# Optimization experiments

Measured on AMD Instinct MI355X. Metric: run time of the kernel, lower is better.

The kernel has to match this reference:

```python
import jax, jax.numpy as jnp
import numpy as np

NUM_EXPERTS = 8
HIDDEN = 2048
INTER = 4096
TOKENS = 4096
TOP_K = 2


def setup_inputs() -> dict:
    key = jax.random.key(0)
    ks = jax.random.split(key, 6)
    x = jax.random.normal(ks[0], (TOKENS, HIDDEN), dtype=jnp.float32)
    expert_weights = jax.random.uniform(ks[1], (TOKENS, TOP_K), dtype=jnp.float32)
    expert_indices = jax.random.randint(ks[2], (TOKENS, TOP_K), 0, NUM_EXPERTS)
    # kaiming_uniform-ish init for stacked expert weights
    b1 = float(np.sqrt(6.0 / HIDDEN))
    b2 = float(np.sqrt(6.0 / INTER))
    w1_stacked = jax.random.uniform(ks[3], (NUM_EXPERTS, HIDDEN, INTER), minval=-b1, maxval=b1, dtype=jnp.float32)
    w2_stacked = jax.random.uniform(ks[4], (NUM_EXPERTS, INTER, HIDDEN), minval=-b2, maxval=b2, dtype=jnp.float32)
    w3_stacked = jax.random.uniform(ks[5], (NUM_EXPERTS, HIDDEN, INTER), minval=-b1, maxval=b1, dtype=jnp.float32)
    return {
        "x": x,
        "expert_weights": expert_weights,
        "w1_stacked": w1_stacked,
        "w2_stacked": w2_stacked,
        "w3_stacked": w3_stacked,
        "expert_indices": expert_indices,
        "num_experts_per_tok": TOP_K,
    }


def reference(x, expert_weights, w1_stacked, w2_stacked, w3_stacked, expert_indices, num_experts_per_tok):
    # out[t] = sum_k expert_weights[t,k] * SwiGLU_FFN_{expert_indices[t,k]}(x[t])
    # Loop over the small fixed expert set; masked weighted combine per expert.
    num_experts = w1_stacked.shape[0]
    out = jnp.zeros_like(x)
    for e in range(num_experts):
        gate = jax.nn.silu(x @ w1_stacked[e])          # [T, I]
        up = x @ w3_stacked[e]                          # [T, I]
        y = (gate * up) @ w2_stacked[e]                 # [T, H]
        # per-token routing weight for expert e (sum over top-k slots)
        w_e = jnp.sum(jnp.where(expert_indices == e, expert_weights, 0.0), axis=1)  # [T]
        out = out + w_e[:, None] * y
    return out
```

## Files before the change

### kernel.cpp

```cpp
#include <hip/hip_runtime.h>
#include <hip/hip_bf16.h>
#include <cstdint>

#define T_TOKENS 4096
#define HID      2048
#define INTER    4096
#define NEXP     8
#define TOPK     2
#define NPAIRS   (T_TOKENS * TOPK)
#define BM 128
#define BN 128
#define BK 32
#define MAXROWS  (NPAIRS + NEXP * BM)
#define NRB1     64

typedef __attribute__((ext_vector_type(8))) short   short8;
typedef __attribute__((ext_vector_type(4))) float   f32x4;
typedef __attribute__((ext_vector_type(8))) ushort  ushort8v;

static __device__ __forceinline__ ushort f2bf(float f) {
    __hip_bfloat16 b = __float2bfloat16(f);
    return __builtin_bit_cast(ushort, b);
}

typedef const __attribute__((address_space(1))) unsigned char ga_u8;
typedef __attribute__((address_space(3))) unsigned char       la_u8;
static __device__ __forceinline__ void gl_lds16(const void* g, void* l) {
    __builtin_amdgcn_global_load_lds((ga_u8*)g, (la_u8*)l, 16, 0, 0);
}

__global__ void route_kernel(const int* __restrict__ eidx,
                             const float* __restrict__ ew,
                             int* __restrict__ cnt, int* __restrict__ pbase,
                             int* __restrict__ tokl, float* __restrict__ wgtl,
                             int* __restrict__ pairrow) {
    __shared__ int s_cnt[NEXP];
    __shared__ int s_pos[NEXP];
    __shared__ int s_base[NEXP];
    int tid = threadIdx.x;
    if (tid < NEXP) { s_cnt[tid] = 0; s_pos[tid] = 0; }
    __syncthreads();
    for (int p = tid; p < NPAIRS; p += blockDim.x)
        atomicAdd(&s_cnt[eidx[p]], 1);
    __syncthreads();
    if (tid == 0) {
        int b = 0;
        for (int e = 0; e < NEXP; ++e) {
            s_base[e] = b;
            cnt[e]    = s_cnt[e];
            pbase[e]  = b;
            b += (s_cnt[e] + BM - 1) / BM * BM;
        }
        pbase[NEXP] = b;
    }
    __syncthreads();
    for (int p = tid; p < NPAIRS; p += blockDim.x) {
        int e   = eidx[p];
        int pos = atomicAdd(&s_pos[e], 1);
        int row = s_base[e] + pos;
        tokl[row]  = p >> 1;
        wgtl[row]  = ew[p];
        pairrow[p] = row;
    }
}

__global__ __launch_bounds__(256) void cvt_x_kernel(const float* __restrict__ x,
                                                    ushort* __restrict__ xbf) {
    int i = (blockIdx.x * 256 + threadIdx.x) * 8;
    float4 a = *reinterpret_cast<const float4*>(x + i);
    float4 b = *reinterpret_cast<const float4*>(x + i + 4);
    ushort8v o;
    o[0] = f2bf(a.x); o[1] = f2bf(a.y); o[2] = f2bf(a.z); o[3] = f2bf(a.w);
    o[4] = f2bf(b.x); o[5] = f2bf(b.y); o[6] = f2bf(b.z); o[7] = f2bf(b.w);
    *reinterpret_cast<ushort8v*>(xbf + i) = o;
}

__global__ __launch_bounds__(256) void transpose_cvt_kernel(
        const float* __restrict__ src, ushort* __restrict__ dst,
        int K, int N, int c0, int CN, long estride) {
    int ez = blockIdx.z;
    const float* s = src + (size_t)ez * estride;
    ushort* d = dst + (size_t)ez * CN * K;
    int nb = blockIdx.x * 64 + c0;
    int kb = blockIdx.y * 64;
    __shared__ ushort t[64][72];
    int tid = threadIdx.x;
    int kr = tid >> 2;
    int ns = tid & 3;
    #pragma unroll
    for (int p = 0; p < 4; ++p) {
        int f = ns + p * 4;
        float4 v = *reinterpret_cast<const float4*>(&s[(size_t)(kb + kr) * N + nb + f * 4]);
        t[f * 4 + 0][kr] = f2bf(v.x);
        t[f * 4 + 1][kr] = f2bf(v.y);
        t[f * 4 + 2][kr] = f2bf(v.z);
        t[f * 4 + 3][kr] = f2bf(v.w);
    }
    __syncthreads();
    int nr = tid >> 2;
    #pragma unroll
    for (int p = 0; p < 2; ++p) {
        int ks = ((tid & 3) + p * 4) * 8;
        ushort8v v8 = *reinterpret_cast<const ushort8v*>(&t[nr][ks]);
        *reinterpret_cast<ushort8v*>(&d[(size_t)(nb - c0 + nr) * K + kb + ks]) = v8;
    }
}

#define SWZV(r) (((r) & 3) ^ (((r) >> 2) & 3))

#define F1_LDSB 24576
__global__ __launch_bounds__(256, 2) void ffn1_kernel(
        const ushort* __restrict__ xbf,
        const ushort* __restrict__ wT1, const ushort* __restrict__ wT3,
        const int* __restrict__ cnt, const int* __restrict__ pbase,
        const int* __restrict__ tokl, ushort* __restrict__ h,
        int e0, int CN, int c0) {
    int d = blockIdx.x;
    int xcd = d & 7, q = d >> 3;
    int gq = q / NRB1, rb = q % NRB1;
    int ncb = CN >> 7;
    int g = gq * 8 + xcd;
    int ez = g / ncb, cb = g - ez * ncb;
    int e = e0 + ez;
    int ce = cnt[e];
    int r0 = rb * BM;
    if (r0 >= ce) return;
    int base = pbase[e];

    __shared__ ushort ldsbuf[2 * F1_LDSB / 2];
    int tid = threadIdx.x, lane = tid & 63, wid = tid >> 6;
    int wr = (wid >> 1) * 64, wc = (wid & 1) * 64;

    int t0 = wid * 32 + (lane >> 2);
    int t1 = t0 + 16;
    int sw0 = (((lane & 3) ^ SWZV(t0)) << 4);
    int sw1 = (((lane & 3) ^ SWZV(t1)) << 4);
    int cr0 = r0 + t0, cr1 = r0 + t1;
    const char* aS0 = (const char*)(xbf + (size_t)tokl[base + (cr0 < ce ? cr0 : 0)] * HID) + sw0;
    const char* aS1 = (const char*)(xbf + (size_t)tokl[base + (cr1 < ce ? cr1 : 0)] * HID) + sw1;
    const ushort* B1g = wT1 + ((size_t)ez * CN + (size_t)cb * 128) * HID;
    const ushort* B3g = wT3 + ((size_t)ez * CN + (size_t)cb * 128) * HID;
    const char* b1S0 = (const char*)(B1g + (size_t)t0 * HID) + sw0;
    const char* b1S1 = (const char*)(B1g + (size_t)t1 * HID) + sw1;
    const char* b3S0 = (const char*)(B3g + (size_t)t0 * HID) + sw0;
    const char* b3S1 = (const char*)(B3g + (size_t)t1 * HID) + sw1;

    char* Lb = (char*)ldsbuf;
    int dst0 = wid * 2048;

    int vl = SWZV(lane & 15);
    int fs = (((lane >> 4) ^ vl) << 4);
    int aoff[4], boff[4];
    #pragma unroll
    for (int i = 0; i < 4; ++i) {
        aoff[i] = (wr + i * 16 + (lane & 15)) * 64 + fs;
        boff[i] = (wc + i * 16 + (lane & 15)) * 64 + fs;
    }

    f32x4 accg[4][4], accu[4][4];
    #pragma unroll
    for (int i = 0; i < 4; ++i)
        #pragma unroll
        for (int j = 0; j < 4; ++j) { accg[i][j] = (f32x4)0.f; accu[i][j] = (f32x4)0.f; }

    auto stage = [&](int buf, int t) {
        char* L = Lb + buf * F1_LDSB;
        int adv = t * 64;
        gl_lds16(aS0 + adv,  L + dst0);
        gl_lds16(aS1 + adv,  L + dst0 + 1024);
        gl_lds16(b1S0 + adv, L + 8192 + dst0);
        gl_lds16(b1S1 + adv, L + 8192 + dst0 + 1024);
        gl_lds16(b3S0 + adv, L + 16384 + dst0);
        gl_lds16(b3S1 + adv, L + 16384 + dst0 + 1024);
    };

    stage(0, 0);
    __syncthreads();
    const int NT = HID / BK;
    for (int t = 0; t < NT; ++t) {
        int cur = t & 1;
        if (t + 1 < NT) stage(cur ^ 1, t + 1);
        const char* L = Lb + cur * F1_LDSB;
        short8 af[4];
        #pragma unroll
        for (int mi = 0; mi < 4; ++mi)
            af[mi] = *reinterpret_cast<const short8*>(L + aoff[mi]);
        #pragma unroll
        for (int ni = 0; ni < 4; ++ni) {
            short8 b1 = *reinterpret_cast<const short8*>(L + 8192 + boff[ni]);
            short8 b3 = *reinterpret_cast<const short8*>(L + 16384 + boff[ni]);
            #pragma unroll
            for (int mi = 0; mi < 4; ++mi) {
                accg[mi][ni] = __builtin_amdgcn_mfma_f32_16x16x32_bf16(af[mi], b1, accg[mi][ni], 0, 0, 0);
                accu[mi][ni] = __builtin_amdgcn_mfma_f32_16x16x32_bf16(af[mi], b3, accu[mi][ni], 0, 0, 0);
            }
        }
        __syncthreads();
    }

    int hcol = c0 + cb * 128 + wc + (lane & 15);
    #pragma unroll
    for (int mi = 0; mi < 4; ++mi) {
        #pragma unroll
        for (int q2 = 0; q2 < 4; ++q2) {
            int r = r0 + wr + mi * 16 + (lane >> 4) * 4 + q2;
            if (r >= ce) continue;
            ushort* hp = h + (size_t)(base + r) * INTER + hcol;
            #pragma unroll
            for (int ni = 0; ni < 4; ++ni) {
                float gg = accg[mi][ni][q2];
                float uu = accu[mi][ni][q2];
                float s = gg / (1.f + __expf(-gg));
                hp[ni * 16] = f2bf(s * uu);
            }
        }
    }
}

#define F2_LDSB 16384
__global__ __launch_bounds__(256, 3) void ffn2_kernel(
        const ushort* __restrict__ h,
        const ushort* __restrict__ wT2,
        const int* __restrict__ cnt, const int* __restrict__ pbase,
        const float* __restrict__ wgtl, ushort* __restrict__ y,
        int e0, int CN, int c0) {
    int d = blockIdx.x;
    int xcd = d & 7, q = d >> 3;
    int gq = q / NRB1, rb = q % NRB1;
    int ncb = CN >> 7;
    int g = gq * 8 + xcd;
    int ez = g / ncb, cb = g - ez * ncb;
    int e = e0 + ez;
    int ce = cnt[e];
    int r0 = rb * BM;
    if (r0 >= ce) return;
    int base = pbase[e];

    __shared__ ushort ldsbuf[2 * F2_LDSB / 2];
    int tid = threadIdx.x, lane = tid & 63, wid = tid >> 6;
    int wr = (wid >> 1) * 64, wc = (wid & 1) * 64;

    int t0 = wid * 32 + (lane >> 2);
    int t1 = t0 + 16;
    int sw0 = (((lane & 3) ^ SWZV(t0)) << 4);
    int sw1 = (((lane & 3) ^ SWZV(t1)) << 4);
    int cr0 = r0 + t0, cr1 = r0 + t1;
    const char* aS0 = (const char*)(h + (size_t)(base + (cr0 < ce ? cr0 : 0)) * INTER) + sw0;
    const char* aS1 = (const char*)(h + (size_t)(base + (cr1 < ce ? cr1 : 0)) * INTER) + sw1;
    const ushort* Bg = wT2 + ((size_t)ez * CN + (size_t)cb * 128) * INTER;
    const char* bS0 = (const char*)(Bg + (size_t)t0 * INTER) + sw0;
    const char* bS1 = (const char*)(Bg + (size_t)t1 * INTER) + sw1;

    char* Lb = (char*)ldsbuf;
    int dst0 = wid * 2048;

    int vl = SWZV(lane & 15);
    int fs = (((lane >> 4) ^ vl) << 4);
    int aoff[4], boff[4];
    #pragma unroll
    for (int i = 0; i < 4; ++i) {
        aoff[i] = (wr + i * 16 + (lane & 15)) * 64 + fs;
        boff[i] = (wc + i * 16 + (lane & 15)) * 64 + fs;
    }

    f32x4 acc[4][4];
    #pragma unroll
    for (int i = 0; i < 4; ++i)
        #pragma unroll
        for (int j = 0; j < 4; ++j) acc[i][j] = (f32x4)0.f;

    auto stage = [&](int buf, int t) {
        char* L = Lb + buf * F2_LDSB;
        int adv = t * 64;
        gl_lds16(aS0 + adv, L + dst0);
        gl_lds16(aS1 + adv, L + dst0 + 1024);
        gl_lds16(bS0 + adv, L + 8192 + dst0);
        gl_lds16(bS1 + adv, L + 8192 + dst0 + 1024);
    };

    stage(0, 0);
    __syncthreads();
    const int NT = INTER / BK;
    for (int t = 0; t < NT; ++t) {
        int cur = t & 1;
        if (t + 1 < NT) stage(cur ^ 1, t + 1);
        const char* L = Lb + cur * F2_LDSB;
        short8 af[4];
        #pragma unroll
        for (int mi = 0; mi < 4; ++mi)
            af[mi] = *reinterpret_cast<const short8*>(L + aoff[mi]);
        #pragma unroll
        for (int ni = 0; ni < 4; ++ni) {
            short8 b = *reinterpret_cast<const short8*>(L + 8192 + boff[ni]);
            #pragma unroll
            for (int mi = 0; mi < 4; ++mi)
                acc[mi][ni] = __builtin_amdgcn_mfma_f32_16x16x32_bf16(af[mi], b, acc[mi][ni], 0, 0, 0);
        }
        __syncthreads();
    }

    int ycol = c0 + cb * 128 + wc + (lane & 15);
    #pragma unroll
    for (int mi = 0; mi < 4; ++mi) {
        #pragma unroll
        for (int q2 = 0; q2 < 4; ++q2) {
            int r = r0 + wr + mi * 16 + (lane >> 4) * 4 + q2;
            if (r >= ce) continue;
            float wv = wgtl[base + r];
            ushort* yp = y + (size_t)(base + r) * HID + ycol;
            #pragma unroll
            for (int ni = 0; ni < 4; ++ni)
                yp[ni * 16] = f2bf(wv * acc[mi][ni][q2]);
        }
    }
}

__global__ __launch_bounds__(256) void combine_kernel(
        const ushort* __restrict__ y, const int* __restrict__ pairrow,
        float* __restrict__ out) {
    int t = blockIdx.x;
    const ushort* y0 = y + (size_t)pairrow[2 * t] * HID;
    const ushort* y1 = y + (size_t)pairrow[2 * t + 1] * HID;
    float* op = out + (size_t)t * HID;
    int c = threadIdx.x * 8;
    uint4 a = *reinterpret_cast<const uint4*>(y0 + c);
    uint4 b = *reinterpret_cast<const uint4*>(y1 + c);
    const uint* au = reinterpret_cast<const uint*>(&a);
    const uint* bu = reinterpret_cast<const uint*>(&b);
    #pragma unroll
    for (int i = 0; i < 4; ++i) {
        float alo = __builtin_bit_cast(float, au[i] << 16);
        float ahi = __builtin_bit_cast(float, au[i] & 0xffff0000u);
        float blo = __builtin_bit_cast(float, bu[i] << 16);
        float bhi = __builtin_bit_cast(float, bu[i] & 0xffff0000u);
        op[c + 2 * i]     = alo + blo;
        op[c + 2 * i + 1] = ahi + bhi;
    }
}

extern "C" void kernel_launch(void* const* d_in, const int* in_sizes, int n_in,
                              void* d_out, int out_size, void* d_ws, size_t ws_size,
                              hipStream_t stream) {
    (void)in_sizes; (void)n_in; (void)out_size;
    const float* x   = (const float*)d_in[0];
    const float* ew  = (const float*)d_in[1];
    const float* w1  = (const float*)d_in[2];
    const float* w2  = (const float*)d_in[3];
    const float* w3  = (const float*)d_in[4];
    const int*  eidx = (const int*)d_in[5];
    float* out = (float*)d_out;

    int*   cnt     = (int*)d_ws;
    int*   pbase   = cnt + 8;
    int*   tokl    = cnt + 32;
    float* wgtl    = (float*)(tokl + MAXROWS);
    int*   pairrow = (int*)(wgtl + MAXROWS);
    ushort* xbf = (ushort*)((((uintptr_t)(pairrow + NPAIRS)) + 255) & ~(uintptr_t)255);
    ushort* h   = xbf + (size_t)T_TOKENS * HID;
    ushort* y   = h + (size_t)MAXROWS * INTER;
    ushort* region = y + (size_t)MAXROWS * HID;
    size_t region_bytes = ws_size - ((char*)region - (char*)d_ws);

    route_kernel<<<1, 256, 0, stream>>>(eidx, ew, cnt, pbase, tokl, wgtl, pairrow);
    cvt_x_kernel<<<T_TOKENS * HID / 8 / 256, 256, 0, stream>>>(x, xbf);

    const size_t per_e1 = (size_t)2 * INTER * HID * 2;
    const size_t per_e2 = (size_t)HID * INTER * 2;

    if (region_bytes >= per_e1) {
        int EG = (int)(region_bytes / per_e1); if (EG > 8) EG = 8;
        for (int g = 0; g < NEXP; g += EG) {
            int ne = (NEXP - g < EG) ? (NEXP - g) : EG;
            ushort* wt1 = region;
            ushort* wt3 = region + (size_t)ne * INTER * HID;
            transpose_cvt_kernel<<<dim3(INTER / 64, HID / 64, ne), 256, 0, stream>>>(
                w1 + (size_t)g * HID * INTER, wt1, HID, INTER, 0, INTER, (long)HID * INTER);
            transpose_cvt_kernel<<<dim3(INTER / 64, HID / 64, ne), 256, 0, stream>>>(
                w3 + (size_t)g * HID * INTER, wt3, HID, INTER, 0, INTER, (long)HID * INTER);
            ffn1_kernel<<<NRB1 * ne * (INTER / BN), 256, 0, stream>>>(
                xbf, wt1, wt3, cnt, pbase, tokl, h, g, INTER, 0);
        }
    } else {
        const int CN = 1024;
        for (int e = 0; e < NEXP; ++e) {
            for (int c = 0; c < INTER; c += CN) {
                ushort* wt1 = region;
                ushort* wt3 = region + (size_t)CN * HID;
                transpose_cvt_kernel<<<dim3(CN / 64, HID / 64, 1), 256, 0, stream>>>(
                    w1 + (size_t)e * HID * INTER, wt1, HID, INTER, c, CN, (long)HID * INTER);
                transpose_cvt_kernel<<<dim3(CN / 64, HID / 64, 1), 256, 0, stream>>>(
                    w3 + (size_t)e * HID * INTER, wt3, HID, INTER, c, CN, (long)HID * INTER);
                ffn1_kernel<<<NRB1 * (CN / BN), 256, 0, stream>>>(
                    xbf, wt1, wt3, cnt, pbase, tokl, h, e, CN, c);
            }
        }
    }

    if (region_bytes >= per_e2) {
        int EG = (int)(region_bytes / per_e2); if (EG > 8) EG = 8;
        for (int g = 0; g < NEXP; g += EG) {
            int ne = (NEXP - g < EG) ? (NEXP - g) : EG;
            ushort* wt2 = region;
            transpose_cvt_kernel<<<dim3(HID / 64, INTER / 64, ne), 256, 0, stream>>>(
                w2 + (size_t)g * INTER * HID, wt2, INTER, HID, 0, HID, (long)INTER * HID);
            ffn2_kernel<<<NRB1 * ne * (HID / BN), 256, 0, stream>>>(
                h, wt2, cnt, pbase, wgtl, y, g, HID, 0);
        }
    } else {
        const int CN = 1024;
        for (int e = 0; e < NEXP; ++e) {
            for (int c = 0; c < HID; c += CN) {
                ushort* wt2 = region;
                transpose_cvt_kernel<<<dim3(CN / 64, INTER / 64, 1), 256, 0, stream>>>(
                    w2 + (size_t)e * INTER * HID, wt2, INTER, HID, c, CN, (long)INTER * HID);
                ffn2_kernel<<<NRB1 * (CN / BN), 256, 0, stream>>>(
                    h, wt2, cnt, pbase, wgtl, y, e, CN, c);
            }
        }
    }

    combine_kernel<<<T_TOKENS, 256, 0, stream>>>(y, pairrow, out);
}
```

Measured before the change: 855.2 us.

## Enlarge MoE GEMM tiles, interleave async loads with MFMA phases, fuse combine via atomics

Both expert GEMM kernels move to 256x128x64 tiles with 512-thread blocks and a larger double-buffered LDS. Global-to-LDS loads for the next k-step are split into chunks placed between MFMA phases, with explicit vmcnt waits, scheduling barriers and s_setprio around the math. The separate combine kernel and y buffer are removed: ffn2 applies the routing weight and atomically adds into the zero-initialised output. This trades more LDS per block (lower occupancy) and float-atomic traffic for better data reuse, better load/compute overlap and one less kernel plus its memory round-trip.

```diff
diff --git a/kernel.cpp b/kernel.cpp
--- a/kernel.cpp
+++ b/kernel.cpp
@@ -8,11 +8,11 @@
 #define NEXP     8
 #define TOPK     2
 #define NPAIRS   (T_TOKENS * TOPK)
-#define BM 128
+#define BM 256
 #define BN 128
-#define BK 32
+#define BK 64
 #define MAXROWS  (NPAIRS + NEXP * BM)
-#define NRB1     64
+#define NRB2     32
 
 typedef __attribute__((ext_vector_type(8))) short   short8;
 typedef __attribute__((ext_vector_type(4))) float   f32x4;
@@ -29,11 +29,17 @@
     __builtin_amdgcn_global_load_lds((ga_u8*)g, (la_u8*)l, 16, 0, 0);
 }
 
+#define SBAR() do { __builtin_amdgcn_sched_barrier(0); \
+                    __builtin_amdgcn_s_barrier(); \
+                    __builtin_amdgcn_sched_barrier(0); \
+                    asm volatile("" ::: "memory"); } while (0)
+#define VMCNT(n) do { asm volatile("s_waitcnt vmcnt(" #n ")" ::: "memory"); \
+                      __builtin_amdgcn_sched_barrier(0); } while (0)
+
 __global__ void route_kernel(const int* __restrict__ eidx,
                              const float* __restrict__ ew,
                              int* __restrict__ cnt, int* __restrict__ pbase,
-                             int* __restrict__ tokl, float* __restrict__ wgtl,
-                             int* __restrict__ pairrow) {
+                             int* __restrict__ tokl, float* __restrict__ wgtl) {
     __shared__ int s_cnt[NEXP];
     __shared__ int s_pos[NEXP];
     __shared__ int s_base[NEXP];
@@ -58,9 +64,8 @@
         int e   = eidx[p];
         int pos = atomicAdd(&s_pos[e], 1);
         int row = s_base[e] + pos;
-        tokl[row]  = p >> 1;
-        wgtl[row]  = ew[p];
-        pairrow[p] = row;
+        tokl[row] = p >> 1;
+        wgtl[row] = ew[p];
     }
 }
 
@@ -106,56 +111,60 @@
     }
 }
 
-#define SWZV(r) (((r) & 3) ^ (((r) >> 2) & 3))
-
-#define F1_LDSB 24576
-__global__ __launch_bounds__(256, 2) void ffn1_kernel(
+__global__ __launch_bounds__(512, 2) void ffn1_kernel(
         const ushort* __restrict__ xbf,
         const ushort* __restrict__ wT1, const ushort* __restrict__ wT3,
         const int* __restrict__ cnt, const int* __restrict__ pbase,
         const int* __restrict__ tokl, ushort* __restrict__ h,
-        int e0, int CN, int c0) {
+        int ncb, int c0) {
     int d = blockIdx.x;
     int xcd = d & 7, q = d >> 3;
-    int gq = q / NRB1, rb = q % NRB1;
-    int ncb = CN >> 7;
+    int gq = q / NRB2, rb = q % NRB2;
     int g = gq * 8 + xcd;
     int ez = g / ncb, cb = g - ez * ncb;
-    int e = e0 + ez;
-    int ce = cnt[e];
+    int ce = cnt[ez];
+    int e = ez;
+    (void)e;
     int r0 = rb * BM;
     if (r0 >= ce) return;
-    int base = pbase[e];
-
-    __shared__ ushort ldsbuf[2 * F1_LDSB / 2];
-    int tid = threadIdx.x, lane = tid & 63, wid = tid >> 6;
+    int base = pbase[ez];
+
+    __shared__ char lds[131072];
+    char* Lb = lds;
+
+    int tid  = threadIdx.x;
+    int lane = tid & 63, wid = tid >> 6;
     int wr = (wid >> 1) * 64, wc = (wid & 1) * 64;
-
-    int t0 = wid * 32 + (lane >> 2);
-    int t1 = t0 + 16;
-    int sw0 = (((lane & 3) ^ SWZV(t0)) << 4);
-    int sw1 = (((lane & 3) ^ SWZV(t1)) << 4);
-    int cr0 = r0 + t0, cr1 = r0 + t1;
-    const char* aS0 = (const char*)(xbf + (size_t)tokl[base + (cr0 < ce ? cr0 : 0)] * HID) + sw0;
-    const char* aS1 = (const char*)(xbf + (size_t)tokl[base + (cr1 < ce ? cr1 : 0)] * HID) + sw1;
-    const ushort* B1g = wT1 + ((size_t)ez * CN + (size_t)cb * 128) * HID;
-    const ushort* B3g = wT3 + ((size_t)ez * CN + (size_t)cb * 128) * HID;
-    const char* b1S0 = (const char*)(B1g + (size_t)t0 * HID) + sw0;
-    const char* b1S1 = (const char*)(B1g + (size_t)t1 * HID) + sw1;
-    const char* b3S0 = (const char*)(B3g + (size_t)t0 * HID) + sw0;
-    const char* b3S1 = (const char*)(B3g + (size_t)t1 * HID) + sw1;
-
-    char* Lb = (char*)ldsbuf;
-    int dst0 = wid * 2048;
-
-    int vl = SWZV(lane & 15);
-    int fs = (((lane >> 4) ^ vl) << 4);
-    int aoff[4], boff[4];
+    int rlow = lane & 15, khi = lane >> 4;
+
+    int rr = tid >> 3;
+    int ss = (tid & 7) ^ (rr & 7);
+    const ushort* pA[4];
     #pragma unroll
     for (int i = 0; i < 4; ++i) {
-        aoff[i] = (wr + i * 16 + (lane & 15)) * 64 + fs;
-        boff[i] = (wc + i * 16 + (lane & 15)) * 64 + fs;
-    }
+        int row = r0 + i * 64 + rr;
+        int tok = (row < ce) ? tokl[base + row] : 0;
+        pA[i] = xbf + (size_t)tok * HID + ss * 8;
+    }
+    size_t wrow = (size_t)ez * ((size_t)ncb * 128) + (size_t)cb * 128;
+    const ushort* pB1[2];
+    const ushort* pB3[2];
+    #pragma unroll
+    for (int i = 0; i < 2; ++i) {
+        pB1[i] = wT1 + (wrow + i * 64 + rr) * HID + ss * 8;
+        pB3[i] = wT3 + (wrow + i * 64 + rr) * HID + ss * 8;
+    }
+    int ldst = wid << 10;
+
+    int aoffs[4][2], boffs[4][2];
+    #pragma unroll
+    for (int mi = 0; mi < 4; ++mi)
+        #pragma unroll
+        for (int kh = 0; kh < 2; ++kh) {
+            int sw = (((kh << 2) + khi) ^ (lane & 7)) << 4;
+            aoffs[mi][kh] = (wr + mi * 16 + rlow) * 128 + sw;
+            boffs[mi][kh] = (wc + mi * 16 + rlow) * 128 + sw;
+        }
 
     f32x4 accg[4][4], accu[4][4];
     #pragma unroll
@@ -163,47 +172,118 @@
         #pragma unroll
         for (int j = 0; j < 4; ++j) { accg[i][j] = (f32x4)0.f; accu[i][j] = (f32x4)0.f; }
 
-    auto stage = [&](int buf, int t) {
-        char* L = Lb + buf * F1_LDSB;
-        int adv = t * 64;
-        gl_lds16(aS0 + adv,  L + dst0);
-        gl_lds16(aS1 + adv,  L + dst0 + 1024);
-        gl_lds16(b1S0 + adv, L + 8192 + dst0);
-        gl_lds16(b1S1 + adv, L + 8192 + dst0 + 1024);
-        gl_lds16(b3S0 + adv, L + 16384 + dst0);
-        gl_lds16(b3S1 + adv, L + 16384 + dst0 + 1024);
-    };
-
-    stage(0, 0);
-    __syncthreads();
+    {
+        char* L = Lb;
+        #pragma unroll
+        for (int i = 0; i < 4; ++i) gl_lds16(pA[i], L + i * 8192 + ldst);
+        #pragma unroll
+        for (int i = 0; i < 2; ++i) gl_lds16(pB1[i], L + 32768 + i * 8192 + ldst);
+        #pragma unroll
+        for (int i = 0; i < 2; ++i) gl_lds16(pB3[i], L + 49152 + i * 8192 + ldst);
+    }
+
     const int NT = HID / BK;
+    #pragma unroll 1
     for (int t = 0; t < NT; ++t) {
-        int cur = t & 1;
-        if (t + 1 < NT) stage(cur ^ 1, t + 1);
-        const char* L = Lb + cur * F1_LDSB;
-        short8 af[4];
+        char* Lc = Lb + ((t & 1) ? 65536 : 0);
+        char* Ln = Lb + ((t & 1) ? 0 : 65536);
+        int adv = (t + 1) * 64;
+        bool more = (t + 1 < NT);
+        if (more) {
+            gl_lds16(pA[0] + adv, Ln + 0 * 8192 + ldst);
+            gl_lds16(pA[1] + adv, Ln + 1 * 8192 + ldst);
+            VMCNT(2);
+        } else {
+            VMCNT(0);
+        }
+        SBAR();
+        short8 af[4][2];
         #pragma unroll
         for (int mi = 0; mi < 4; ++mi)
-            af[mi] = *reinterpret_cast<const short8*>(L + aoff[mi]);
-        #pragma unroll
-        for (int ni = 0; ni < 4; ++ni) {
-            short8 b1 = *reinterpret_cast<const short8*>(L + 8192 + boff[ni]);
-            short8 b3 = *reinterpret_cast<const short8*>(L + 16384 + boff[ni]);
-            #pragma unroll
-            for (int mi = 0; mi < 4; ++mi) {
-                accg[mi][ni] = __builtin_amdgcn_mfma_f32_16x16x32_bf16(af[mi], b1, accg[mi][ni], 0, 0, 0);
-                accu[mi][ni] = __builtin_amdgcn_mfma_f32_16x16x32_bf16(af[mi], b3, accu[mi][ni], 0, 0, 0);
-            }
-        }
-        __syncthreads();
-    }
-
-    int hcol = c0 + cb * 128 + wc + (lane & 15);
+            #pragma unroll
+            for (int kh = 0; kh < 2; ++kh)
+                af[mi][kh] = *reinterpret_cast<const short8*>(Lc + aoffs[mi][kh]);
+        short8 bf[2][2];
+        #pragma unroll
+        for (int ni = 0; ni < 2; ++ni)
+            #pragma unroll
+            for (int kh = 0; kh < 2; ++kh)
+                bf[ni][kh] = *reinterpret_cast<const short8*>(Lc + 32768 + boffs[ni][kh]);
+        if (more) {
+            gl_lds16(pA[2] + adv, Ln + 2 * 8192 + ldst);
+            gl_lds16(pA[3] + adv, Ln + 3 * 8192 + ldst);
+        }
+        __builtin_amdgcn_s_setprio(1);
+        #pragma unroll
+        for (int ni = 0; ni < 2; ++ni)
+            #pragma unroll
+            for (int mi = 0; mi < 4; ++mi)
+                #pragma unroll
+                for (int kh = 0; kh < 2; ++kh)
+                    accg[mi][ni] = __builtin_amdgcn_mfma_f32_16x16x32_bf16(af[mi][kh], bf[ni][kh], accg[mi][ni], 0, 0, 0);
+        __builtin_amdgcn_s_setprio(0);
+        SBAR();
+        #pragma unroll
+        for (int ni = 0; ni < 2; ++ni)
+            #pragma unroll
+            for (int kh = 0; kh < 2; ++kh)
+                bf[ni][kh] = *reinterpret_cast<const short8*>(Lc + 49152 + boffs[ni][kh]);
+        if (more) {
+            gl_lds16(pB1[0] + adv, Ln + 32768 + ldst);
+            gl_lds16(pB1[1] + adv, Ln + 32768 + 8192 + ldst);
+        }
+        __builtin_amdgcn_s_setprio(1);
+        #pragma unroll
+        for (int ni = 0; ni < 2; ++ni)
+            #pragma unroll
+            for (int mi = 0; mi < 4; ++mi)
+                #pragma unroll
+                for (int kh = 0; kh < 2; ++kh)
+                    accu[mi][ni] = __builtin_amdgcn_mfma_f32_16x16x32_bf16(af[mi][kh], bf[ni][kh], accu[mi][ni], 0, 0, 0);
+        __builtin_amdgcn_s_setprio(0);
+        SBAR();
+        #pragma unroll
+        for (int ni = 0; ni < 2; ++ni)
+            #pragma unroll
+            for (int kh = 0; kh < 2; ++kh)
+                bf[ni][kh] = *reinterpret_cast<const short8*>(Lc + 32768 + boffs[ni + 2][kh]);
+        if (more) {
+            gl_lds16(pB3[0] + adv, Ln + 49152 + ldst);
+            gl_lds16(pB3[1] + adv, Ln + 49152 + 8192 + ldst);
+        }
+        __builtin_amdgcn_s_setprio(1);
+        #pragma unroll
+        for (int ni = 0; ni < 2; ++ni)
+            #pragma unroll
+            for (int mi = 0; mi < 4; ++mi)
+                #pragma unroll
+                for (int kh = 0; kh < 2; ++kh)
+                    accg[mi][ni + 2] = __builtin_amdgcn_mfma_f32_16x16x32_bf16(af[mi][kh], bf[ni][kh], accg[mi][ni + 2], 0, 0, 0);
+        __builtin_amdgcn_s_setprio(0);
+        SBAR();
+        #pragma unroll
+        for (int ni = 0; ni < 2; ++ni)
+            #pragma unroll
+            for (int kh = 0; kh < 2; ++kh)
+                bf[ni][kh] = *reinterpret_cast<const short8*>(Lc + 49152 + boffs[ni + 2][kh]);
+        __builtin_amdgcn_s_setprio(1);
+        #pragma unroll
+        for (int ni = 0; ni < 2; ++ni)
+            #pragma unroll
+            for (int mi = 0; mi < 4; ++mi)
+                #pragma unroll
+                for (int kh = 0; kh < 2; ++kh)
+                    accu[mi][ni + 2] = __builtin_amdgcn_mfma_f32_16x16x32_bf16(af[mi][kh], bf[ni][kh], accu[mi][ni + 2], 0, 0, 0);
+        __builtin_amdgcn_s_setprio(0);
+        SBAR();
+    }
+
+    int hcol = c0 + cb * 128 + wc + rlow;
     #pragma unroll
     for (int mi = 0; mi < 4; ++mi) {
         #pragma unroll
         for (int q2 = 0; q2 < 4; ++q2) {
-            int r = r0 + wr + mi * 16 + (lane >> 4) * 4 + q2;
+            int r = r0 + wr + mi * 16 + khi * 4 + q2;
             if (r >= ce) continue;
             ushort* hp = h + (size_t)(base + r) * INTER + hcol;
             #pragma unroll
@@ -217,51 +297,52 @@
     }
 }
 
-#define F2_LDSB 16384
-__global__ __launch_bounds__(256, 3) void ffn2_kernel(
+__global__ __launch_bounds__(512, 2) void ffn2_kernel(
         const ushort* __restrict__ h,
         const ushort* __restrict__ wT2,
         const int* __restrict__ cnt, const int* __restrict__ pbase,
-        const float* __restrict__ wgtl, ushort* __restrict__ y,
-        int e0, int CN, int c0) {
+        const int* __restrict__ tokl, const float* __restrict__ wgtl,
+        float* __restrict__ out, int ncb, int c0) {
     int d = blockIdx.x;
     int xcd = d & 7, q = d >> 3;
-    int gq = q / NRB1, rb = q % NRB1;
-    int ncb = CN >> 7;
+    int gq = q / NRB2, rb = q % NRB2;
     int g = gq * 8 + xcd;
     int ez = g / ncb, cb = g - ez * ncb;
-    int e = e0 + ez;
-    int ce = cnt[e];
+    int ce = cnt[ez];
     int r0 = rb * BM;
     if (r0 >= ce) return;
-    int base = pbase[e];
-
-    __shared__ ushort ldsbuf[2 * F2_LDSB / 2];
-    int tid = threadIdx.x, lane = tid & 63, wid = tid >> 6;
+    int base = pbase[ez];
+
+    __shared__ char lds[98304];
+    char* Lb = lds;
+
+    int tid  = threadIdx.x;
+    int lane = tid & 63, wid = tid >> 6;
     int wr = (wid >> 1) * 64, wc = (wid & 1) * 64;
-
-    int t0 = wid * 32 + (lane >> 2);
-    int t1 = t0 + 16;
-    int sw0 = (((lane & 3) ^ SWZV(t0)) << 4);
-    int sw1 = (((lane & 3) ^ SWZV(t1)) << 4);
-    int cr0 = r0 + t0, cr1 = r0 + t1;
-    const char* aS0 = (const char*)(h + (size_t)(base + (cr0 < ce ? cr0 : 0)) * INTER) + sw0;
-    const char* aS1 = (const char*)(h + (size_t)(base + (cr1 < ce ? cr1 : 0)) * INTER) + sw1;
-    const ushort* Bg = wT2 + ((size_t)ez * CN + (size_t)cb * 128) * INTER;
-    const char* bS0 = (const char*)(Bg + (size_t)t0 * INTER) + sw0;
-    const char* bS1 = (const char*)(Bg + (size_t)t1 * INTER) + sw1;
-
-    char* Lb = (char*)ldsbuf;
-    int dst0 = wid * 2048;
-
-    int vl = SWZV(lane & 15);
-    int fs = (((lane >> 4) ^ vl) << 4);
-    int aoff[4], boff[4];
-    #pragma unroll
-    for (int i = 0; i < 4; ++i) {
-        aoff[i] = (wr + i * 16 + (lane & 15)) * 64 + fs;
-        boff[i] = (wc + i * 16 + (lane & 15)) * 64 + fs;
-    }
+    int rlow = lane & 15, khi = lane >> 4;
+
+    int rr = tid >> 3;
+    int ss = (tid & 7) ^ (rr & 7);
+    const ushort* pA[4];
+    #pragma unroll
+    for (int i = 0; i < 4; ++i)
+        pA[i] = h + (size_t)(base + r0 + i * 64 + rr) * INTER + ss * 8;
+    size_t wrow = (size_t)ez * ((size_t)ncb * 128) + (size_t)cb * 128;
+    const ushort* pB[2];
+    #pragma unroll
+    for (int i = 0; i < 2; ++i)
+        pB[i] = wT2 + (wrow + i * 64 + rr) * INTER + ss * 8;
+    int ldst = wid << 10;
+
+    int aoffs[4][2], boffs[4][2];
+    #pragma unroll
+    for (int mi = 0; mi < 4; ++mi)
+        #pragma unroll
+        for (int kh = 0; kh < 2; ++kh) {
+            int sw = (((kh << 2) + khi) ^ (lane & 7)) << 4;
+            aoffs[mi][kh] = (wr + mi * 16 + rlow) * 128 + sw;
+            boffs[mi][kh] = (wc + mi * 16 + rlow) * 128 + sw;
+        }
 
     f32x4 acc[4][4];
     #pragma unroll
@@ -269,72 +350,90 @@
         #pragma unroll
         for (int j = 0; j < 4; ++j) acc[i][j] = (f32x4)0.f;
 
-    auto stage = [&](int buf, int t) {
-        char* L = Lb + buf * F2_LDSB;
-        int adv = t * 64;
-        gl_lds16(aS0 + adv, L + dst0);
-        gl_lds16(aS1 + adv, L + dst0 + 1024);
-        gl_lds16(bS0 + adv, L + 8192 + dst0);
-        gl_lds16(bS1 + adv, L + 8192 + dst0 + 1024);
-    };
-
-    stage(0, 0);
-    __syncthreads();
+    {
+        char* L = Lb;
+        #pragma unroll
+        for (int i = 0; i < 4; ++i) gl_lds16(pA[i], L + i * 8192 + ldst);
+        #pragma unroll
+        for (int i = 0; i < 2; ++i) gl_lds16(pB[i], L + 32768 + i * 8192 + ldst);
+    }
+
     const int NT = INTER / BK;
+    #pragma unroll 1
     for (int t = 0; t < NT; ++t) {
-        int cur = t & 1;
-        if (t + 1 < NT) stage(cur ^ 1, t + 1);
-        const char* L = Lb + cur * F2_LDSB;
-        short8 af[4];
+        char* Lc = Lb + ((t & 1) ? 49152 : 0);
+        char* Ln = Lb + ((t & 1) ? 0 : 49152);
+        int adv = (t + 1) * 64;
+        bool more = (t + 1 < NT);
+        if (more) {
+            gl_lds16(pA[0] + adv, Ln + 0 * 8192 + ldst);
+            gl_lds16(pA[1] + adv, Ln + 1 * 8192 + ldst);
+            VMCNT(2);
+        } else {
+            VMCNT(0);
+        }
+        SBAR();
+        short8 af[4][2];
         #pragma unroll
         for (int mi = 0; mi < 4; ++mi)
-            af[mi] = *reinterpret_cast<const short8*>(L + aoff[mi]);
-        #pragma unroll
-        for (int ni = 0; ni < 4; ++ni) {
-            short8 b = *reinterpret_cast<const short8*>(L + 8192 + boff[ni]);
+            #pragma unroll
+            for (int kh = 0; kh < 2; ++kh)
+                af[mi][kh] = *reinterpret_cast<const short8*>(Lc + aoffs[mi][kh]);
+        short8 bf[2][2];
+        #pragma unroll
+        for (int ni = 0; ni < 2; ++ni)
+            #pragma unroll
+            for (int kh = 0; kh < 2; ++kh)
+                bf[ni][kh] = *reinterpret_cast<const short8*>(Lc + 32768 + boffs[ni][kh]);
+        if (more) {
+            gl_lds16(pA[2] + adv, Ln + 2 * 8192 + ldst);
+            gl_lds16(pA[3] + adv, Ln + 3 * 8192 + ldst);
+        }
+        __builtin_amdgcn_s_setprio(1);
+        #pragma unroll
+        for (int ni = 0; ni < 2; ++ni)
             #pragma unroll
             for (int mi = 0; mi < 4; ++mi)
-                acc[mi][ni] = __builtin_amdgcn_mfma_f32_16x16x32_bf16(af[mi], b, acc[mi][ni], 0, 0, 0);
-        }
-        __syncthreads();
-    }
-
-    int ycol = c0 + cb * 128 + wc + (lane & 15);
+                #pragma unroll
+                for (int kh = 0; kh < 2; ++kh)
+                    acc[mi][ni] = __builtin_amdgcn_mfma_f32_16x16x32_bf16(af[mi][kh], bf[ni][kh], acc[mi][ni], 0, 0, 0);
+        __builtin_amdgcn_s_setprio(0);
+        SBAR();
+        #pragma unroll
+        for (int ni = 0; ni < 2; ++ni)
+            #pragma unroll
+            for (int kh = 0; kh < 2; ++kh)
+                bf[ni][kh] = *reinterpret_cast<const short8*>(Lc + 32768 + boffs[ni + 2][kh]);
+        if (more) {
+            gl_lds16(pB[0] + adv, Ln + 32768 + ldst);
+            gl_lds16(pB[1] + adv, Ln + 32768 + 8192 + ldst);
+        }
+        __builtin_amdgcn_s_setprio(1);
+        #pragma unroll
+        for (int ni = 0; ni < 2; ++ni)
+            #pragma unroll
+            for (int mi = 0; mi < 4; ++mi)
+                #pragma unroll
+                for (int kh = 0; kh < 2; ++kh)
+                    acc[mi][ni + 2] = __builtin_amdgcn_mfma_f32_16x16x32_bf16(af[mi][kh], bf[ni][kh], acc[mi][ni + 2], 0, 0, 0);
+        __builtin_amdgcn_s_setprio(0);
+        SBAR();
+    }
+
+    int ocol = c0 + cb * 128 + wc + rlow;
     #pragma unroll
     for (int mi = 0; mi < 4; ++mi) {
         #pragma unroll
         for (int q2 = 0; q2 < 4; ++q2) {
-            int r = r0 + wr + mi * 16 + (lane >> 4) * 4 + q2;
+            int r = r0 + wr + mi * 16 + khi * 4 + q2;
             if (r >= ce) continue;
+            int tok  = tokl[base + r];
             float wv = wgtl[base + r];
-            ushort* yp = y + (size_t)(base + r) * HID + ycol;
+            float* op = out + (size_t)tok * HID + ocol;
             #pragma unroll
             for (int ni = 0; ni < 4; ++ni)
-                yp[ni * 16] = f2bf(wv * acc[mi][ni][q2]);
-        }
-    }
-}
-
-__global__ __launch_bounds__(256) void combine_kernel(
-        const ushort* __restrict__ y, const int* __restrict__ pairrow,
-        float* __restrict__ out) {
-    int t = blockIdx.x;
-    const ushort* y0 = y + (size_t)pairrow[2 * t] * HID;
-    const ushort* y1 = y + (size_t)pairrow[2 * t + 1] * HID;
-    float* op = out + (size_t)t * HID;
-    int c = threadIdx.x * 8;
-    uint4 a = *reinterpret_cast<const uint4*>(y0 + c);
-    uint4 b = *reinterpret_cast<const uint4*>(y1 + c);
-    const uint* au = reinterpret_cast<const uint*>(&a);
-    const uint* bu = reinterpret_cast<const uint*>(&b);
-    #pragma unroll
-    for (int i = 0; i < 4; ++i) {
-        float alo = __builtin_bit_cast(float, au[i] << 16);
-        float ahi = __builtin_bit_cast(float, au[i] & 0xffff0000u);
-        float blo = __builtin_bit_cast(float, bu[i] << 16);
-        float bhi = __builtin_bit_cast(float, bu[i] & 0xffff0000u);
-        op[c + 2 * i]     = alo + blo;
-        op[c + 2 * i + 1] = ahi + bhi;
+                atomicAdd(&op[ni * 16], wv * acc[mi][ni][q2]);
+        }
     }
 }
 
@@ -350,18 +449,17 @@
     const int*  eidx = (const int*)d_in[5];
     float* out = (float*)d_out;
 
-    int*   cnt     = (int*)d_ws;
-    int*   pbase   = cnt + 8;
-    int*   tokl    = cnt + 32;
-    float* wgtl    = (float*)(tokl + MAXROWS);
-    int*   pairrow = (int*)(wgtl + MAXROWS);
-    ushort* xbf = (ushort*)((((uintptr_t)(pairrow + NPAIRS)) + 255) & ~(uintptr_t)255);
-    ushort* h   = xbf + (size_t)T_TOKENS * HID;
-    ushort* y   = h + (size_t)MAXROWS * INTER;
-    ushort* region = y + (size_t)MAXROWS * HID;
+    int*   cnt   = (int*)d_ws;
+    int*   pbase = cnt + 8;
+    int*   tokl  = cnt + 32;
+    float* wgtl  = (float*)(tokl + MAXROWS);
+    ushort* xbf  = (ushort*)((((uintptr_t)(wgtl + MAXROWS)) + 255) & ~(uintptr_t)255);
+    ushort* h    = xbf + (size_t)T_TOKENS * HID;
+    ushort* region = h + (size_t)MAXROWS * INTER;
     size_t region_bytes = ws_size - ((char*)region - (char*)d_ws);
 
-    route_kernel<<<1, 256, 0, stream>>>(eidx, ew, cnt, pbase, tokl, wgtl, pairrow);
+    hipMemsetAsync(d_out, 0, (size_t)T_TOKENS * HID * sizeof(float), stream);
+    route_kernel<<<1, 256, 0, stream>>>(eidx, ew, cnt, pbase, tokl, wgtl);
     cvt_x_kernel<<<T_TOKENS * HID / 8 / 256, 256, 0, stream>>>(x, xbf);
 
     const size_t per_e1 = (size_t)2 * INTER * HID * 2;
@@ -377,8 +475,8 @@
                 w1 + (size_t)g * HID * INTER, wt1, HID, INTER, 0, INTER, (long)HID * INTER);
             transpose_cvt_kernel<<<dim3(INTER / 64, HID / 64, ne), 256, 0, stream>>>(
                 w3 + (size_t)g * HID * INTER, wt3, HID, INTER, 0, INTER, (long)HID * INTER);
-            ffn1_kernel<<<NRB1 * ne * (INTER / BN), 256, 0, stream>>>(
-                xbf, wt1, wt3, cnt, pbase, tokl, h, g, INTER, 0);
+            ffn1_kernel<<<NRB2 * ne * (INTER / BN), 512, 0, stream>>>(
+                xbf, wt1, wt3, cnt + g, pbase + g, tokl, h, INTER / BN, 0);
         }
     } else {
         const int CN = 1024;
@@ -390,8 +488,8 @@
                     w1 + (size_t)e * HID * INTER, wt1, HID, INTER, c, CN, (long)HID * INTER);
                 transpose_cvt_kernel<<<dim3(CN / 64, HID / 64, 1), 256, 0, stream>>>(
                     w3 + (size_t)e * HID * INTER, wt3, HID, INTER, c, CN, (long)HID * INTER);
-                ffn1_kernel<<<NRB1 * (CN / BN), 256, 0, stream>>>(
-                    xbf, wt1, wt3, cnt, pbase, tokl, h, e, CN, c);
+                ffn1_kernel<<<NRB2 * (CN / BN), 512, 0, stream>>>(
+                    xbf, wt1, wt3, cnt + e, pbase + e, tokl, h, CN / BN, c);
             }
         }
     }
@@ -403,8 +501,8 @@
             ushort* wt2 = region;
             transpose_cvt_kernel<<<dim3(HID / 64, INTER / 64, ne), 256, 0, stream>>>(
                 w2 + (size_t)g * INTER * HID, wt2, INTER, HID, 0, HID, (long)INTER * HID);
-            ffn2_kernel<<<NRB1 * ne * (HID / BN), 256, 0, stream>>>(
-                h, wt2, cnt, pbase, wgtl, y, g, HID, 0);
+            ffn2_kernel<<<NRB2 * ne * (HID / BN), 512, 0, stream>>>(
+                h, wt2, cnt + g, pbase + g, tokl, wgtl, out, HID / BN, 0);
         }
     } else {
         const int CN = 1024;
@@ -413,11 +511,9 @@
                 ushort* wt2 = region;
                 transpose_cvt_kernel<<<dim3(CN / 64, INTER / 64, 1), 256, 0, stream>>>(
                     w2 + (size_t)e * INTER * HID, wt2, INTER, HID, c, CN, (long)INTER * HID);
-                ffn2_kernel<<<NRB1 * (CN / BN), 256, 0, stream>>>(
-                    h, wt2, cnt, pbase, wgtl, y, e, CN, c);
+                ffn2_kernel<<<NRB2 * (CN / BN), 512, 0, stream>>>(
+                    h, wt2, cnt + e, pbase + e, tokl, wgtl, out, CN / BN, c);
             }
         }
     }
-
-    combine_kernel<<<T_TOKENS, 256, 0, stream>>>(y, pairrow, out);
-}
+}
```

New measurement: 873.0 us. 2.1% more time.

## Overlap weight transpose-convert with FFN1 using idle blocks as persistent workers

Applied to the files above, without the earlier changes.

Idle ffn1 blocks, meaning row tiles beyond an expert's token count, now pull weight-transpose tiles from an atomic work counter. They prefetch the next expert pair's w1/w3 into a double buffer and convert w2 for the current pair. The FFN1 stage runs in four two-expert steps with ping-pong buffers, and all experts' w2 is converted ahead so a single ffn2 launch covers all eight experts. This hides the fp32-to-bf16 transpose traffic behind GEMM work and cuts launch count, at the cost of a larger workspace and contention between the transposes and the GEMM for bandwidth. The fallback path drops the chunked-CN mode.

```diff
diff --git a/kernel.cpp b/kernel.cpp
--- a/kernel.cpp
+++ b/kernel.cpp
@@ -32,6 +32,7 @@
 __global__ void route_kernel(const int* __restrict__ eidx,
                              const float* __restrict__ ew,
                              int* __restrict__ cnt, int* __restrict__ pbase,
+                             int* __restrict__ ctrs,
                              int* __restrict__ tokl, float* __restrict__ wgtl,
                              int* __restrict__ pairrow) {
     __shared__ int s_cnt[NEXP];
@@ -39,6 +40,7 @@
     __shared__ int s_base[NEXP];
     int tid = threadIdx.x;
     if (tid < NEXP) { s_cnt[tid] = 0; s_pos[tid] = 0; }
+    if (tid < 8) ctrs[tid] = 0;
     __syncthreads();
     for (int p = tid; p < NPAIRS; p += blockDim.x)
         atomicAdd(&s_cnt[eidx[p]], 1);
@@ -75,15 +77,10 @@
     *reinterpret_cast<ushort8v*>(xbf + i) = o;
 }
 
-__global__ __launch_bounds__(256) void transpose_cvt_kernel(
-        const float* __restrict__ src, ushort* __restrict__ dst,
-        int K, int N, int c0, int CN, long estride) {
-    int ez = blockIdx.z;
-    const float* s = src + (size_t)ez * estride;
-    ushort* d = dst + (size_t)ez * CN * K;
-    int nb = blockIdx.x * 64 + c0;
-    int kb = blockIdx.y * 64;
-    __shared__ ushort t[64][72];
+static __device__ void trans_tile(const float* __restrict__ s, ushort* __restrict__ d,
+                                  int K, int N, int tile, ushort (*t)[72]) {
+    int nb = (tile % (N >> 6)) << 6;
+    int kb = (tile / (N >> 6)) << 6;
     int tid = threadIdx.x;
     int kr = tid >> 2;
     int ns = tid & 3;
@@ -102,8 +99,18 @@
     for (int p = 0; p < 2; ++p) {
         int ks = ((tid & 3) + p * 4) * 8;
         ushort8v v8 = *reinterpret_cast<const ushort8v*>(&t[nr][ks]);
-        *reinterpret_cast<ushort8v*>(&d[(size_t)(nb - c0 + nr) * K + kb + ks]) = v8;
-    }
+        *reinterpret_cast<ushort8v*>(&d[(size_t)(nb + nr) * K + kb + ks]) = v8;
+    }
+    __syncthreads();
+}
+
+__global__ __launch_bounds__(256) void transpose_cvt_kernel(
+        const float* __restrict__ src, ushort* __restrict__ dst,
+        int K, int N, long estride) {
+    __shared__ ushort t[64][72];
+    int ez = blockIdx.z;
+    trans_tile(src + (size_t)ez * estride, dst + (size_t)ez * (size_t)N * K,
+               K, N, blockIdx.y * (N >> 6) + blockIdx.x, t);
 }
 
 #define SWZV(r) (((r) & 3) ^ (((r) >> 2) & 3))
@@ -114,7 +121,15 @@
         const ushort* __restrict__ wT1, const ushort* __restrict__ wT3,
         const int* __restrict__ cnt, const int* __restrict__ pbase,
         const int* __restrict__ tokl, ushort* __restrict__ h,
-        int e0, int CN, int c0) {
+        int e0, int CN, int c0,
+        const float* __restrict__ j1w1, const float* __restrict__ j1w3,
+        ushort* __restrict__ j1dst, int j1ne,
+        const float* __restrict__ j2src, ushort* __restrict__ j2dst, int j2ne,
+        int* __restrict__ ctr) {
+    __shared__ ushort ldsbuf[2 * F1_LDSB / 2];
+    __shared__ ushort tw[64][72];
+    __shared__ int s_id;
+
     int d = blockIdx.x;
     int xcd = d & 7, q = d >> 3;
     int gq = q / NRB1, rb = q % NRB1;
@@ -124,11 +139,34 @@
     int e = e0 + ez;
     int ce = cnt[e];
     int r0 = rb * BM;
-    if (r0 >= ce) return;
+    int tid = threadIdx.x;
+    if (r0 >= ce) {
+        const int tpm = (HID >> 6) * (INTER >> 6);
+        int n1 = j1ne * 2 * tpm;
+        int n2 = j2ne * tpm;
+        int tot = n1 + n2;
+        if (tot == 0) return;
+        for (;;) {
+            if (tid == 0) s_id = atomicAdd(ctr, 1);
+            __syncthreads();
+            int id = s_id;
+            if (id >= tot) return;
+            if (id < n1) {
+                int m = id / tpm, r = id % tpm;
+                const float* src = (m < j1ne ? j1w1 + (size_t)m * HID * INTER
+                                             : j1w3 + (size_t)(m - j1ne) * HID * INTER);
+                trans_tile(src, j1dst + (size_t)m * INTER * HID, HID, INTER, r, tw);
+            } else {
+                int id2 = id - n1;
+                int m = id2 / tpm, r = id2 % tpm;
+                trans_tile(j2src + (size_t)m * INTER * HID,
+                           j2dst + (size_t)m * (size_t)HID * INTER, INTER, HID, r, tw);
+            }
+        }
+    }
     int base = pbase[e];
 
-    __shared__ ushort ldsbuf[2 * F1_LDSB / 2];
-    int tid = threadIdx.x, lane = tid & 63, wid = tid >> 6;
+    int lane = tid & 63, wid = tid >> 6;
     int wr = (wid >> 1) * 64, wc = (wid & 1) * 64;
 
     int t0 = wid * 32 + (lane >> 2);
@@ -352,6 +390,7 @@
 
     int*   cnt     = (int*)d_ws;
     int*   pbase   = cnt + 8;
+    int*   ctrs    = cnt + 20;
     int*   tokl    = cnt + 32;
     float* wgtl    = (float*)(tokl + MAXROWS);
     int*   pairrow = (int*)(wgtl + MAXROWS);
@@ -361,62 +400,65 @@
     ushort* region = y + (size_t)MAXROWS * HID;
     size_t region_bytes = ws_size - ((char*)region - (char*)d_ws);
 
-    route_kernel<<<1, 256, 0, stream>>>(eidx, ew, cnt, pbase, tokl, wgtl, pairrow);
+    const size_t IH = (size_t)INTER * HID;
+    const long   ES = (long)HID * INTER;
+
+    route_kernel<<<1, 256, 0, stream>>>(eidx, ew, cnt, pbase, ctrs, tokl, wgtl, pairrow);
     cvt_x_kernel<<<T_TOKENS * HID / 8 / 256, 256, 0, stream>>>(x, xbf);
 
-    const size_t per_e1 = (size_t)2 * INTER * HID * 2;
-    const size_t per_e2 = (size_t)HID * INTER * 2;
-
-    if (region_bytes >= per_e1) {
-        int EG = (int)(region_bytes / per_e1); if (EG > 8) EG = 8;
-        for (int g = 0; g < NEXP; g += EG) {
-            int ne = (NEXP - g < EG) ? (NEXP - g) : EG;
+    const size_t GRP = 4 * IH * sizeof(ushort);
+    const size_t WC  = 8 * IH * sizeof(ushort);
+
+    if (region_bytes >= 2 * GRP + WC) {
+        ushort* bufA = region;
+        ushort* bufB = region + 4 * IH;
+        ushort* bufC = region + 8 * IH;
+
+        transpose_cvt_kernel<<<dim3(INTER / 64, HID / 64, 2), 256, 0, stream>>>(
+            w1, bufA, HID, INTER, ES);
+        transpose_cvt_kernel<<<dim3(INTER / 64, HID / 64, 2), 256, 0, stream>>>(
+            w3, bufA + 2 * IH, HID, INTER, ES);
+
+        for (int s = 0; s < 4; ++s) {
+            int e0 = 2 * s;
+            ushort* buf = (s & 1) ? bufB : bufA;
+            ushort* nxt = (s & 1) ? bufA : bufB;
+            int j1ne = (s < 3) ? 2 : 0;
+            const float* j1w1 = w1 + (size_t)(e0 + 2) * IH;
+            const float* j1w3 = w3 + (size_t)(e0 + 2) * IH;
+            const float* j2s  = w2 + (size_t)e0 * IH;
+            ushort* j2d = bufC + (size_t)e0 * IH;
+            ffn1_kernel<<<NRB1 * 2 * (INTER / BN), 256, 0, stream>>>(
+                xbf, buf, buf + 2 * IH, cnt, pbase, tokl, h, e0, INTER, 0,
+                j1w1, j1w3, nxt, j1ne, j2s, j2d, 2, ctrs + s);
+        }
+        ffn2_kernel<<<NRB1 * 8 * (HID / BN), 256, 0, stream>>>(
+            h, bufC, cnt, pbase, wgtl, y, 0, HID, 0);
+    } else {
+        const size_t per_e1 = 2 * IH * sizeof(ushort);
+        const size_t per_e2 = IH * sizeof(ushort);
+        int EG1 = (int)(region_bytes / per_e1); if (EG1 > 8) EG1 = 8; if (EG1 < 1) EG1 = 1;
+        for (int g = 0; g < NEXP; g += EG1) {
+            int ne = (NEXP - g < EG1) ? (NEXP - g) : EG1;
             ushort* wt1 = region;
-            ushort* wt3 = region + (size_t)ne * INTER * HID;
+            ushort* wt3 = region + (size_t)ne * IH;
             transpose_cvt_kernel<<<dim3(INTER / 64, HID / 64, ne), 256, 0, stream>>>(
-                w1 + (size_t)g * HID * INTER, wt1, HID, INTER, 0, INTER, (long)HID * INTER);
+                w1 + (size_t)g * IH, wt1, HID, INTER, ES);
             transpose_cvt_kernel<<<dim3(INTER / 64, HID / 64, ne), 256, 0, stream>>>(
-                w3 + (size_t)g * HID * INTER, wt3, HID, INTER, 0, INTER, (long)HID * INTER);
+                w3 + (size_t)g * IH, wt3, HID, INTER, ES);
             ffn1_kernel<<<NRB1 * ne * (INTER / BN), 256, 0, stream>>>(
-                xbf, wt1, wt3, cnt, pbase, tokl, h, g, INTER, 0);
-        }
-    } else {
-        const int CN = 1024;
-        for (int e = 0; e < NEXP; ++e) {
-            for (int c = 0; c < INTER; c += CN) {
-                ushort* wt1 = region;
-                ushort* wt3 = region + (size_t)CN * HID;
-                transpose_cvt_kernel<<<dim3(CN / 64, HID / 64, 1), 256, 0, stream>>>(
-                    w1 + (size_t)e * HID * INTER, wt1, HID, INTER, c, CN, (long)HID * INTER);
-                transpose_cvt_kernel<<<dim3(CN / 64, HID / 64, 1), 256, 0, stream>>>(
-                    w3 + (size_t)e * HID * INTER, wt3, HID, INTER, c, CN, (long)HID * INTER);
-                ffn1_kernel<<<NRB1 * (CN / BN), 256, 0, stream>>>(
-                    xbf, wt1, wt3, cnt, pbase, tokl, h, e, CN, c);
-            }
-        }
-    }
-
-    if (region_bytes >= per_e2) {
-        int EG = (int)(region_bytes / per_e2); if (EG > 8) EG = 8;
-        for (int g = 0; g < NEXP; g += EG) {
-            int ne = (NEXP - g < EG) ? (NEXP - g) : EG;
+                xbf, wt1, wt3, cnt, pbase, tokl, h, g, INTER, 0,
+                w1, w3, region, 0, w2, region, 0, ctrs + 7);
+        }
+        int EG2 = (int)(region_bytes / per_e2); if (EG2 > 8) EG2 = 8; if (EG2 < 1) EG2 = 1;
+        for (int g = 0; g < NEXP; g += EG2) {
+            int ne = (NEXP - g < EG2) ? (NEXP - g) : EG2;
             ushort* wt2 = region;
             transpose_cvt_kernel<<<dim3(HID / 64, INTER / 64, ne), 256, 0, stream>>>(
-                w2 + (size_t)g * INTER * HID, wt2, INTER, HID, 0, HID, (long)INTER * HID);
+                w2 + (size_t)g * IH, wt2, INTER, HID, ES);
             ffn2_kernel<<<NRB1 * ne * (HID / BN), 256, 0, stream>>>(
                 h, wt2, cnt, pbase, wgtl, y, g, HID, 0);
         }
-    } else {
-        const int CN = 1024;
-        for (int e = 0; e < NEXP; ++e) {
-            for (int c = 0; c < HID; c += CN) {
-                ushort* wt2 = region;
-                transpose_cvt_kernel<<<dim3(CN / 64, INTER / 64, 1), 256, 0, stream>>>(
-                    w2 + (size_t)e * INTER * HID, wt2, INTER, HID, c, CN, (long)INTER * HID);
-                ffn2_kernel<<<NRB1 * (CN / BN), 256, 0, stream>>>(
-                    h, wt2, cnt, pbase, wgtl, y, e, CN, c);
-            }
-        }
     }
 
     combine_kernel<<<T_TOKENS, 256, 0, stream>>>(y, pairrow, out);
```

Result: slower. 1.387 ms (+62.1%).
